# Kernel tuning notes

Measured on AMD Instinct MI355X. Metric: run time of the kernel, lower is better.

The kernel has to match this reference:

```python
import jax, jax.numpy as jnp
from jax import lax
import numpy as np

B, M = 16384, 200            # flattened batch (B*TT), tokens per observation
NUM_LAYERS, GW, GH = 22, 11, 11
CNN_CH, HIDDEN = 128, 512
ACTION_NVEC = (9, 10)

MAX_VEC = jnp.array([9.0, 1.0, 1.0, 10.0, 3.0, 254.0, 1.0, 1.0, 235.0, 8.0, 9.0,
                     250.0, 29.0, 1.0, 1.0, 8.0, 1.0, 1.0, 6.0, 3.0, 1.0, 2.0],
                    jnp.float32)[None, :, None, None]  # [1,22,1,1]


def setup_inputs() -> dict:
    key = jax.random.key(0)
    ks = jax.random.split(key, 16)
    # compose coords byte so x,y nibbles are valid grid indices (0..10)
    xs = jax.random.randint(ks[0], (B, M), 0, GW)
    ys = jax.random.randint(ks[1], (B, M), 0, GH)
    coords = xs * 16 + ys
    atr = jax.random.randint(ks[2], (B, M), 0, NUM_LAYERS)
    val = jax.random.randint(ks[3], (B, M), 0, 11)
    observations = jnp.stack([coords, atr, val], axis=-1).astype(jnp.int32)  # [B,M,3]

    def nrm(k, shape, std=0.02):
        return (jax.random.normal(k, shape, jnp.float32) * std)

    return {
        "observations": observations,
        "conv1_w": nrm(ks[4], (CNN_CH, NUM_LAYERS, 5, 5)),
        "conv1_b": jnp.zeros((CNN_CH,), jnp.float32),
        "conv2_w": nrm(ks[5], (CNN_CH, CNN_CH, 3, 3)),
        "conv2_b": jnp.zeros((CNN_CH,), jnp.float32),
        "fc_w": nrm(ks[6], (HIDDEN // 2, CNN_CH)),
        "fc_b": jnp.zeros((HIDDEN // 2,), jnp.float32),
        "self_w": nrm(ks[7], (HIDDEN // 2, NUM_LAYERS)),
        "self_b": jnp.zeros((HIDDEN // 2,), jnp.float32),
        "actor0_w": nrm(ks[8], (ACTION_NVEC[0], HIDDEN), std=0.01),
        "actor0_b": jnp.zeros((ACTION_NVEC[0],), jnp.float32),
        "actor1_w": nrm(ks[9], (ACTION_NVEC[1], HIDDEN), std=0.01),
        "actor1_b": jnp.zeros((ACTION_NVEC[1],), jnp.float32),
        "value_w": nrm(ks[10], (1, HIDDEN)),
        "value_b": jnp.zeros((1,), jnp.float32),
    }


def reference(observations, conv1_w, conv1_b, conv2_w, conv2_b, fc_w, fc_b,
              self_w, self_b, actor0_w, actor0_b, actor1_w, actor1_b,
              value_w, value_b):
    obs = jnp.where(observations == 255, 0, observations)
    coords = obs[..., 0]
    xs = (coords >> 4) & 15
    ys = coords & 15
    atr = obs[..., 1]
    vals = obs[..., 2].astype(jnp.float32)           # [B,M]
    Bt = obs.shape[0]
    b_idx = jnp.broadcast_to(jnp.arange(Bt)[:, None], vals.shape)
    # masked scatter into dense grid (all tokens valid after 255->0 clamp)
    box = jnp.zeros((Bt, NUM_LAYERS, GW, GH), jnp.float32)
    box = box.at[b_idx, atr, xs, ys].set(vals, mode="drop")
    feats = box / MAX_VEC                            # [B,22,11,11]

    self_f = jax.nn.relu(feats[:, :, 5, 5] @ self_w.T + self_b)  # [B,256]

    dn = ("NCHW", "OIHW", "NCHW")
    h = lax.conv_general_dilated(feats, conv1_w, (3, 3), "VALID", dimension_numbers=dn)
    h = jax.nn.relu(h + conv1_b[None, :, None, None])            # [B,128,3,3]
    h = lax.conv_general_dilated(h, conv2_w, (1, 1), "VALID", dimension_numbers=dn)
    h = jax.nn.relu(h + conv2_b[None, :, None, None])            # [B,128,1,1]
    h = h.reshape(Bt, -1)
    cnn_f = jax.nn.relu(h @ fc_w.T + fc_b)                       # [B,256]

    hidden = jnp.concatenate([self_f, cnn_f], axis=1)            # [B,512]
    logits0 = hidden @ actor0_w.T + actor0_b
    logits1 = hidden @ actor1_w.T + actor1_b
    value = hidden @ value_w.T + value_b
    return (logits0, logits1, value)
```

## Files before the change

kernel.cpp:

```cpp
#include <hip/hip_runtime.h>

typedef unsigned short u16;
typedef __attribute__((ext_vector_type(8))) short short8;
typedef __attribute__((ext_vector_type(4))) float f32x4;

#define MFMA16(a, b, c) __builtin_amdgcn_mfma_f32_16x16x32_bf16((a), (b), (c), 0, 0, 0)

__device__ __forceinline__ u16 f2bf(float f) {
    unsigned u = __float_as_uint(f);
    unsigned r = (u + 0x7FFFu + ((u >> 16) & 1u)) >> 16;
    return (u16)r;
}

__device__ const float MAXV[22] = {9.f, 1.f, 1.f, 10.f, 3.f, 254.f, 1.f, 1.f, 235.f, 8.f, 9.f,
                                   250.f, 29.f, 1.f, 1.f, 8.f, 1.f, 1.f, 6.f, 3.f, 1.f, 2.f};

__global__ void prep_kernel(
    const float* c1w, const float* c1b, const float* c2w, const float* c2b,
    const float* fcw, const float* fcb, const float* sfw, const float* sfb,
    const float* a0w, const float* a0b, const float* a1w, const float* a1b,
    const float* vw, const float* vb,
    u16* W1F, u16* W2F, u16* FCF, u16* SELFF, u16* HEADF, float* BIAS)
{
    int idx = blockIdx.x * 256 + threadIdx.x;
    if (idx < 73728) {
        int grp = idx >> 9, off = idx & 511;
        int g = grp / 18, ks = grp - g * 18;
        int l = off >> 3, e = off & 7;
        int n = g * 16 + (l & 15);
        int k = ks * 32 + ((l >> 4) << 3) + e;
        float v = 0.f;
        if (k < 550) { int c = k / 25; v = c1w[n * 550 + k] * (1.0f / MAXV[c]); }
        W1F[idx] = f2bf(v);
    } else if (idx < 221184) {
        int j = idx - 73728;
        int grp = j >> 9, off = j & 511;
        int g = grp / 36, ks = grp - g * 36;
        int l = off >> 3, e = off & 7;
        int oc = g * 16 + (l & 15);
        int k = ks * 32 + ((l >> 4) << 3) + e;
        W2F[j] = f2bf(c2w[oc * 1152 + (k & 127) * 9 + (k >> 7)]);
    } else if (idx < 253952) {
        int j = idx - 221184;
        int grp = j >> 9, off = j & 511;
        int g = grp >> 2, kc = grp & 3;
        int l = off >> 3, e = off & 7;
        int n = g * 16 + (l & 15);
        int k = kc * 32 + ((l >> 4) << 3) + e;
        FCF[j] = f2bf(fcw[n * 128 + k]);
    } else if (idx < 262144) {
        int j = idx - 253952;
        int g = j >> 9, off = j & 511;
        int l = off >> 3, e = off & 7;
        int n = g * 16 + (l & 15);
        int k = ((l >> 4) << 3) + e;
        float v = (k < 22) ? sfw[n * 22 + k] * (1.0f / MAXV[k]) : 0.f;
        SELFF[j] = f2bf(v);
    } else if (idx < 278528) {
        int j = idx - 262144;
        int grp = j >> 9, off = j & 511;
        int g = grp >> 4, ks = grp & 15;
        int l = off >> 3, e = off & 7;
        int n = g * 16 + (l & 15);
        int k = ks * 32 + ((l >> 4) << 3) + e;
        float v = 0.f;
        if (n < 9) v = a0w[n * 512 + k];
        else if (n < 19) v = a1w[(n - 9) * 512 + k];
        else if (n == 19) v = vw[k];
        HEADF[j] = f2bf(v);
    } else if (idx < 279328) {
        int j = idx - 278528;
        float v = 0.f;
        if (j < 128) v = c1b[j];
        else if (j < 256) v = c2b[j - 128];
        else if (j < 512) v = fcb[j - 256];
        else if (j < 768) v = sfb[j - 512];
        else {
            int j2 = j - 768;
            if (j2 < 9) v = a0b[j2]; else if (j2 < 19) v = a1b[j2 - 9]; else if (j2 == 19) v = vb[0];
        }
        BIAS[j] = v;
    }
}

__global__ __launch_bounds__(256, 3) void k12_kernel(
    const int* __restrict__ obs, const u16* __restrict__ W1F,
    const float* __restrict__ BIAS, u16* __restrict__ h1F, u16* __restrict__ s22g)
{
    __shared__ __align__(16) u16 Ablk[4 * 5328];
    __shared__ u16 s22[128];
    const int tid = threadIdx.x, w = tid >> 6, l = tid & 63;
    const int s0 = blockIdx.x * 4;
    const short8 z8 = {0, 0, 0, 0, 0, 0, 0, 0};

    const int* myobs = obs + (long)(s0 + w) * 600;
    int tk[4][3];
    #pragma unroll
    for (int r = 0; r < 4; ++r) {
        int m = r * 64 + l; m = m < 200 ? m : 0;
        tk[r][0] = myobs[m * 3]; tk[r][1] = myobs[m * 3 + 1]; tk[r][2] = myobs[m * 3 + 2];
    }
    if (l < 32) s22[w * 32 + l] = 0;

    u16* blk = Ablk + w * 5328;
    for (int i = l; i < 666; i += 64) *(short8*)(blk + i * 8) = z8;

    int* boxW = (int*)blk;
    int ce[4], en[4], ok[4], va[4], xa[4], ya[4], aa[4], win[4];
    #pragma unroll
    for (int r = 0; r < 4; ++r) {
        int m = r * 64 + l;
        int c = tk[r][0], a = tk[r][1], v = tk[r][2];
        c = (c == 255) ? 0 : c; a = (a == 255) ? 0 : a; v = (v == 255) ? 0 : v;
        int xs = (c >> 4) & 15, ys = c & 15;
        ok[r] = (m < 200) & ((unsigned)a < 22u) & (xs < 11) & (ys < 11);
        ce[r] = ok[r] ? (a * 121 + xs * 11 + ys) : 0;
        en[r] = ((m + 1) << 8) | (v & 255);
        va[r] = v; xa[r] = xs; ya[r] = ys; aa[r] = a;
        if (ok[r]) atomicMax(&boxW[ce[r]], en[r]);
    }
    __builtin_amdgcn_sched_barrier(0);
    #pragma unroll
    for (int r = 0; r < 4; ++r) win[r] = ok[r] & (boxW[ce[r]] == en[r]);
    __builtin_amdgcn_sched_barrier(0);
    for (int i = l; i < 666; i += 64) *(short8*)(blk + i * 8) = z8;
    __builtin_amdgcn_sched_barrier(0);
    #pragma unroll
    for (int r = 0; r < 4; ++r) {
        if (win[r]) {
            u16 bv = f2bf((float)va[r]);
            if (xa[r] == 5 && ya[r] == 5) s22[w * 32 + aa[r]] = bv;
            int bcol = aa[r] * 25;
            #pragma unroll
            for (int ox = 0; ox < 3; ++ox) {
                int kx = xa[r] - 3 * ox;
                if ((unsigned)kx > 4u) continue;
                #pragma unroll
                for (int oy = 0; oy < 3; ++oy) {
                    int ky = ya[r] - 3 * oy;
                    if ((unsigned)ky > 4u) continue;
                    int pos = ox * 3 + oy;
                    int row = w * 9 + pos;
                    int off = (((pos * 576 + bcol + kx * 5 + ky)) << 1) ^ ((row & 7) << 4);
                    *(u16*)((char*)blk + off) = bv;
                }
            }
        }
    }
    if (l < 32) s22g[(s0 + w) * 32 + l] = s22[w * 32 + l];
    __syncthreads();

    int addr[3][2];
    #pragma unroll
    for (int mt = 0; mt < 3; ++mt) {
        int row = mt * 16 + (l & 15);
        row = row < 36 ? row : 35;
        int ls = row / 9, pos = row - ls * 9;
        int koff = (l >> 4) << 3;
        addr[mt][0] = ls * 10656 + (((pos * 576 + koff) << 1) ^ ((row & 7) << 4));
        addr[mt][1] = ls * 10656 + (((pos * 576 + 32 + koff) << 1) ^ ((row & 7) << 4));
    }
    const u16* Wp0 = W1F + ((w * 2 + 0) * 18 << 9) + l * 8;
    const u16* Wp1 = W1F + ((w * 2 + 1) * 18 << 9) + l * 8;

    f32x4 acc[3][2];
    const f32x4 fz = {0.f, 0.f, 0.f, 0.f};
    #pragma unroll
    for (int i = 0; i < 3; ++i) { acc[i][0] = fz; acc[i][1] = fz; }

    short8 cb0 = *(const short8*)(Wp0);
    short8 cb1 = *(const short8*)(Wp1);
    short8 nb0 = *(const short8*)(Wp0 + 512);
    short8 nb1 = *(const short8*)(Wp1 + 512);
    __builtin_amdgcn_s_setprio(1);
    #pragma unroll
    for (int ks = 0; ks < 18; ++ks) {
        short8 t0 = cb0, t1 = cb1;
        if (ks < 16) {
            t0 = *(const short8*)(Wp0 + (ks + 2) * 512);
            t1 = *(const short8*)(Wp1 + (ks + 2) * 512);
        }
        short8 a0 = *(const short8*)((const char*)Ablk + addr[0][ks & 1] + (ks >> 1) * 128);
        short8 a1 = *(const short8*)((const char*)Ablk + addr[1][ks & 1] + (ks >> 1) * 128);
        short8 a2 = *(const short8*)((const char*)Ablk + addr[2][ks & 1] + (ks >> 1) * 128);
        acc[0][0] = MFMA16(a0, cb0, acc[0][0]);
        acc[0][1] = MFMA16(a0, cb1, acc[0][1]);
        acc[1][0] = MFMA16(a1, cb0, acc[1][0]);
        acc[1][1] = MFMA16(a1, cb1, acc[1][1]);
        acc[2][0] = MFMA16(a2, cb0, acc[2][0]);
        acc[2][1] = MFMA16(a2, cb1, acc[2][1]);
        cb0 = nb0; cb1 = nb1; nb0 = t0; nb1 = t1;
    }
    __builtin_amdgcn_s_setprio(0);
    __syncthreads();

    u16* R = Ablk;
    #pragma unroll
    for (int mt = 0; mt < 3; ++mt) {
        #pragma unroll
        for (int nt = 0; nt < 2; ++nt) {
            int col = w * 32 + nt * 16 + (l & 15);
            float bias = BIAS[col];
            int hif = nt * 2 + ((l & 15) >> 3);
            int ef = l & 7;
            #pragma unroll
            for (int r = 0; r < 4; ++r) {
                int row = mt * 16 + ((l >> 4) << 2) + r;
                if (row < 36) {
                    int ds = row / 9;
                    int pos = row - ds * 9;
                    int ks = pos * 4 + w;
                    float v = acc[mt][nt][r] + bias;
                    v = v > 0.f ? v : 0.f;
                    R[(ks * 16 + hif * 4 + ds) * 8 + ef] = f2bf(v);
                }
            }
        }
    }
    __syncthreads();
    {
        const long Cbase = (long)(s0 >> 4) * 18432 + (s0 & 15) * 8;
        #pragma unroll
        for (int q = 0; q < 3; ++q) {
            int slot = tid + q * 256;
            if (slot < 576) {
                int ks = slot >> 4, lf = slot & 15;
                *(short8*)(h1F + Cbase + ks * 512 + (lf >> 2) * 128 + (lf & 3) * 8) =
                    *(const short8*)(R + slot * 8);
            }
        }
    }
}

__global__ __launch_bounds__(256, 4) void k3_kernel(
    const u16* __restrict__ h1F, const u16* __restrict__ s22g,
    const u16* __restrict__ W2F, const u16* __restrict__ FCF,
    const u16* __restrict__ SELFF, const u16* __restrict__ HEADF,
    const float* __restrict__ BIAS, float* __restrict__ out, int B)
{
    __shared__ __align__(16) u16 A3[16 * 136];
    __shared__ __align__(16) u16 HID[16 * 520];
    const int tid = threadIdx.x, w = tid >> 6, l = tid & 63;
    const int s0 = blockIdx.x * 16;
    const float* c2b = BIAS + 128;
    const float* fcb = BIAS + 256;
    const float* sfb = BIAS + 512;
    const float* hdb = BIAS + 768;
    const f32x4 fz = {0.f, 0.f, 0.f, 0.f};

    const u16* Ap  = h1F + (long)blockIdx.x * 18432 + l * 8;
    const u16* B0p = W2F + ((w * 2 + 0) * 36 << 9) + l * 8;
    const u16* B1p = W2F + ((w * 2 + 1) * 36 << 9) + l * 8;
    f32x4 acc0 = fz, acc1 = fz;
    short8 pa[3], pb0[3], pb1[3];
    #pragma unroll
    for (int d = 0; d < 3; ++d) {
        pa[d]  = *(const short8*)(Ap + d * 512);
        pb0[d] = *(const short8*)(B0p + d * 512);
        pb1[d] = *(const short8*)(B1p + d * 512);
    }
    __builtin_amdgcn_s_setprio(1);
    #pragma unroll
    for (int g = 0; g < 12; ++g) {
        #pragma unroll
        for (int d = 0; d < 3; ++d) {
            int ks = g * 3 + d;
            short8 a = pa[d], b0 = pb0[d], b1 = pb1[d];
            if (ks < 33) {
                pa[d]  = *(const short8*)(Ap + (ks + 3) * 512);
                pb0[d] = *(const short8*)(B0p + (ks + 3) * 512);
                pb1[d] = *(const short8*)(B1p + (ks + 3) * 512);
            }
            acc0 = MFMA16(a, b0, acc0);
            acc1 = MFMA16(a, b1, acc1);
        }
    }
    __builtin_amdgcn_s_setprio(0);
    {
        #pragma unroll
        for (int nt = 0; nt < 2; ++nt) {
            int col = w * 32 + nt * 16 + (l & 15);
            float bias = c2b[col];
            const f32x4& a4 = nt ? acc1 : acc0;
            #pragma unroll
            for (int r = 0; r < 4; ++r) {
                int row = ((l >> 4) << 2) + r;
                float v = a4[r] + bias; v = v > 0.f ? v : 0.f;
                A3[row * 136 + col] = f2bf(v);
            }
        }
    }
    __syncthreads();

    f32x4 acc8[4];
    #pragma unroll
    for (int j = 0; j < 4; ++j) acc8[j] = fz;
    #pragma unroll
    for (int kc = 0; kc < 4; ++kc) {
        short8 bf[4];
        #pragma unroll
        for (int nt = 0; nt < 4; ++nt)
            bf[nt] = *(const short8*)(FCF + (((w * 4 + nt) * 4 + kc) << 9) + l * 8);
        short8 a = *(const short8*)(A3 + (l & 15) * 136 + kc * 32 + ((l >> 4) << 3));
        #pragma unroll
        for (int nt = 0; nt < 4; ++nt) acc8[nt] = MFMA16(a, bf[nt], acc8[nt]);
    }
    #pragma unroll
    for (int nt = 0; nt < 4; ++nt) {
        int col = w * 64 + nt * 16 + (l & 15);
        float bias = fcb[col];
        #pragma unroll
        for (int r = 0; r < 4; ++r) {
            int row = ((l >> 4) << 2) + r;
            float v = acc8[nt][r] + bias; v = v > 0.f ? v : 0.f;
            HID[row * 520 + 256 + col] = f2bf(v);
        }
    }

    {
        f32x4 acc9[4];
        #pragma unroll
        for (int j = 0; j < 4; ++j) acc9[j] = fz;
        short8 bs[4];
        #pragma unroll
        for (int nt = 0; nt < 4; ++nt)
            bs[nt] = *(const short8*)(SELFF + ((w * 4 + nt) << 9) + l * 8);
        short8 a = *(const short8*)(s22g + (s0 + (l & 15)) * 32 + ((l >> 4) << 3));
        #pragma unroll
        for (int nt = 0; nt < 4; ++nt) acc9[nt] = MFMA16(a, bs[nt], acc9[nt]);
        #pragma unroll
        for (int nt = 0; nt < 4; ++nt) {
            int col = w * 64 + nt * 16 + (l & 15);
            float bias = sfb[col];
            #pragma unroll
            for (int r = 0; r < 4; ++r) {
                int row = ((l >> 4) << 2) + r;
                float v = acc9[nt][r] + bias; v = v > 0.f ? v : 0.f;
                HID[row * 520 + col] = f2bf(v);
            }
        }
    }
    __syncthreads();

    if (w < 2) {
        f32x4 hacc = fz;
        #pragma unroll
        for (int ks = 0; ks < 16; ++ks) {
            short8 a = *(const short8*)(HID + (l & 15) * 520 + ks * 32 + ((l >> 4) << 3));
            short8 b = *(const short8*)(HEADF + ((w * 16 + ks) << 9) + l * 8);
            hacc = MFMA16(a, b, hacc);
        }
        #pragma unroll
        for (int r = 0; r < 4; ++r) {
            int srow = s0 + ((l >> 4) << 2) + r;
            int col = w * 16 + (l & 15);
            float v = hacc[r] + hdb[col];
            if (col < 9) out[(long)srow * 9 + col] = v;
            else if (col < 19) out[(long)B * 9 + (long)srow * 10 + (col - 9)] = v;
            else if (col == 19) out[(long)B * 19 + srow] = v;
        }
    }
}

extern "C" void kernel_launch(void* const* d_in, const int* in_sizes, int n_in,
                              void* d_out, int out_size, void* d_ws, size_t ws_size,
                              hipStream_t stream)
{
    const int*   obs = (const int*)d_in[0];
    const float* c1w = (const float*)d_in[1];
    const float* c1b = (const float*)d_in[2];
    const float* c2w = (const float*)d_in[3];
    const float* c2b = (const float*)d_in[4];
    const float* fcw = (const float*)d_in[5];
    const float* fcb = (const float*)d_in[6];
    const float* sfw = (const float*)d_in[7];
    const float* sfb = (const float*)d_in[8];
    const float* a0w = (const float*)d_in[9];
    const float* a0b = (const float*)d_in[10];
    const float* a1w = (const float*)d_in[11];
    const float* a1b = (const float*)d_in[12];
    const float* vw  = (const float*)d_in[13];
    const float* vb  = (const float*)d_in[14];
    const int B = in_sizes[0] / 600;

    char* ws = (char*)d_ws;
    u16*   W1F   = (u16*)(ws + 0);
    u16*   W2F   = (u16*)(ws + 147456);
    u16*   FCF   = (u16*)(ws + 442368);
    u16*   SELFF = (u16*)(ws + 507904);
    u16*   HEADF = (u16*)(ws + 524288);
    float* BIAS  = (float*)(ws + 557056);
    u16*   s22g  = (u16*)(ws + 560256);
    u16*   h1F   = (u16*)(ws + 560256 + (size_t)B * 64);

    prep_kernel<<<1092, 256, 0, stream>>>(c1w, c1b, c2w, c2b, fcw, fcb, sfw, sfb,
                                          a0w, a0b, a1w, a1b, vw, vb,
                                          W1F, W2F, FCF, SELFF, HEADF, BIAS);
    k12_kernel<<<B / 4, 256, 0, stream>>>(obs, W1F, BIAS, h1F, s22g);
    k3_kernel<<<B / 16, 256, 0, stream>>>(h1F, s22g, W2F, FCF, SELFF, HEADF, BIAS,
                                          (float*)d_out, B);
}
```

Before: 79.31 us.

## Persist conv1 weights in registers across samples and split conv2 into its own kernel

The conv1 kernel now handles 16 samples per block in a four-iteration loop. It keeps all of its B-fragment weights in registers (36 short8) instead of re-streaming them per block, and prefetches the next group's observations. Outputs go straight to global memory with scattered 2-byte stores rather than through an LDS staging pass. Conv2 moves into a new kernel that processes 32 samples per block so each weight load is reused twice, and its output goes to a global buffer that a third kernel reads for the FC and head layers. This adds a kernel launch and a global round-trip, and the higher register pressure lowers the occupancy target to 2.

```diff
diff --git a/kernel.cpp b/kernel.cpp
--- a/kernel.cpp
+++ b/kernel.cpp
@@ -83,72 +83,26 @@
     }
 }
 
-__global__ __launch_bounds__(256, 3) void k12_kernel(
+__global__ __launch_bounds__(256, 2) void k12_kernel(
     const int* __restrict__ obs, const u16* __restrict__ W1F,
     const float* __restrict__ BIAS, u16* __restrict__ h1F, u16* __restrict__ s22g)
 {
     __shared__ __align__(16) u16 Ablk[4 * 5328];
     __shared__ u16 s22[128];
     const int tid = threadIdx.x, w = tid >> 6, l = tid & 63;
-    const int s0 = blockIdx.x * 4;
+    const int sbase = blockIdx.x * 16;
     const short8 z8 = {0, 0, 0, 0, 0, 0, 0, 0};
-
-    const int* myobs = obs + (long)(s0 + w) * 600;
-    int tk[4][3];
-    #pragma unroll
-    for (int r = 0; r < 4; ++r) {
-        int m = r * 64 + l; m = m < 200 ? m : 0;
-        tk[r][0] = myobs[m * 3]; tk[r][1] = myobs[m * 3 + 1]; tk[r][2] = myobs[m * 3 + 2];
-    }
-    if (l < 32) s22[w * 32 + l] = 0;
-
     u16* blk = Ablk + w * 5328;
-    for (int i = l; i < 666; i += 64) *(short8*)(blk + i * 8) = z8;
-
     int* boxW = (int*)blk;
-    int ce[4], en[4], ok[4], va[4], xa[4], ya[4], aa[4], win[4];
-    #pragma unroll
-    for (int r = 0; r < 4; ++r) {
-        int m = r * 64 + l;
-        int c = tk[r][0], a = tk[r][1], v = tk[r][2];
-        c = (c == 255) ? 0 : c; a = (a == 255) ? 0 : a; v = (v == 255) ? 0 : v;
-        int xs = (c >> 4) & 15, ys = c & 15;
-        ok[r] = (m < 200) & ((unsigned)a < 22u) & (xs < 11) & (ys < 11);
-        ce[r] = ok[r] ? (a * 121 + xs * 11 + ys) : 0;
-        en[r] = ((m + 1) << 8) | (v & 255);
-        va[r] = v; xa[r] = xs; ya[r] = ys; aa[r] = a;
-        if (ok[r]) atomicMax(&boxW[ce[r]], en[r]);
-    }
-    __builtin_amdgcn_sched_barrier(0);
-    #pragma unroll
-    for (int r = 0; r < 4; ++r) win[r] = ok[r] & (boxW[ce[r]] == en[r]);
-    __builtin_amdgcn_sched_barrier(0);
-    for (int i = l; i < 666; i += 64) *(short8*)(blk + i * 8) = z8;
-    __builtin_amdgcn_sched_barrier(0);
-    #pragma unroll
-    for (int r = 0; r < 4; ++r) {
-        if (win[r]) {
-            u16 bv = f2bf((float)va[r]);
-            if (xa[r] == 5 && ya[r] == 5) s22[w * 32 + aa[r]] = bv;
-            int bcol = aa[r] * 25;
-            #pragma unroll
-            for (int ox = 0; ox < 3; ++ox) {
-                int kx = xa[r] - 3 * ox;
-                if ((unsigned)kx > 4u) continue;
-                #pragma unroll
-                for (int oy = 0; oy < 3; ++oy) {
-                    int ky = ya[r] - 3 * oy;
-                    if ((unsigned)ky > 4u) continue;
-                    int pos = ox * 3 + oy;
-                    int row = w * 9 + pos;
-                    int off = (((pos * 576 + bcol + kx * 5 + ky)) << 1) ^ ((row & 7) << 4);
-                    *(u16*)((char*)blk + off) = bv;
-                }
-            }
-        }
-    }
-    if (l < 32) s22g[(s0 + w) * 32 + l] = s22[w * 32 + l];
-    __syncthreads();
+
+    short8 bfr[36];
+    #pragma unroll
+    for (int nt = 0; nt < 2; ++nt)
+        #pragma unroll
+        for (int ks = 0; ks < 18; ++ks)
+            bfr[nt * 18 + ks] = *(const short8*)(W1F + (((w * 2 + nt) * 18 + ks) << 9) + l * 8);
+    #pragma unroll
+    for (int i = 0; i < 36; ++i) asm volatile("" : "+v"(bfr[i]));
 
     int addr[3][2];
     #pragma unroll
@@ -160,150 +114,214 @@
         addr[mt][0] = ls * 10656 + (((pos * 576 + koff) << 1) ^ ((row & 7) << 4));
         addr[mt][1] = ls * 10656 + (((pos * 576 + 32 + koff) << 1) ^ ((row & 7) << 4));
     }
-    const u16* Wp0 = W1F + ((w * 2 + 0) * 18 << 9) + l * 8;
-    const u16* Wp1 = W1F + ((w * 2 + 1) * 18 << 9) + l * 8;
-
-    f32x4 acc[3][2];
+    const int col0 = w * 32 + (l & 15);
+    const float bias0 = BIAS[col0], bias1 = BIAS[col0 + 16];
+
+    int tkc[4][3], tkn[4][3];
+    {
+        const int* myobs = obs + (long)(sbase + w) * 600;
+        #pragma unroll
+        for (int r = 0; r < 4; ++r) {
+            int m = r * 64 + l; m = m < 200 ? m : 0;
+            tkc[r][0] = myobs[m * 3]; tkc[r][1] = myobs[m * 3 + 1]; tkc[r][2] = myobs[m * 3 + 2];
+        }
+    }
+
+    #pragma clang loop unroll(disable)
+    for (int it = 0; it < 4; ++it) {
+        const int s0it = sbase + it * 4;
+        for (int i = l; i < 666; i += 64) *(short8*)(blk + i * 8) = z8;
+        if (l < 32) s22[w * 32 + l] = 0;
+        int ce[4], en[4], okm = 0;
+        #pragma unroll
+        for (int r = 0; r < 4; ++r) {
+            int m = r * 64 + l;
+            int c = tkc[r][0], a = tkc[r][1], v = tkc[r][2];
+            c = (c == 255) ? 0 : c; a = (a == 255) ? 0 : a; v = (v == 255) ? 0 : v;
+            int xs = (c >> 4) & 15, ys = c & 15;
+            int ok = (m < 200) & ((unsigned)a < 22u) & (xs < 11) & (ys < 11);
+            okm |= ok << r;
+            ce[r] = ok ? (a * 121 + xs * 11 + ys) : 0;
+            en[r] = ((m + 1) << 8) | (v & 255);
+            if (ok) atomicMax(&boxW[ce[r]], en[r]);
+        }
+        __builtin_amdgcn_sched_barrier(0);
+        int winm = 0;
+        #pragma unroll
+        for (int r = 0; r < 4; ++r)
+            if (((okm >> r) & 1) && boxW[ce[r]] == en[r]) winm |= 1 << r;
+        __builtin_amdgcn_sched_barrier(0);
+        for (int i = l; i < 666; i += 64) *(short8*)(blk + i * 8) = z8;
+        __builtin_amdgcn_sched_barrier(0);
+        #pragma unroll
+        for (int r = 0; r < 4; ++r) {
+            if ((winm >> r) & 1) {
+                int c = tkc[r][0], a = tkc[r][1], v = tkc[r][2];
+                c = (c == 255) ? 0 : c; a = (a == 255) ? 0 : a; v = (v == 255) ? 0 : v;
+                int xs = (c >> 4) & 15, ys = c & 15;
+                u16 bv = f2bf((float)v);
+                if (xs == 5 && ys == 5) s22[w * 32 + a] = bv;
+                int bcol = a * 25;
+                #pragma unroll
+                for (int ox = 0; ox < 3; ++ox) {
+                    int kx = xs - 3 * ox;
+                    if ((unsigned)kx > 4u) continue;
+                    #pragma unroll
+                    for (int oy = 0; oy < 3; ++oy) {
+                        int ky = ys - 3 * oy;
+                        if ((unsigned)ky > 4u) continue;
+                        int pos = ox * 3 + oy;
+                        int row = w * 9 + pos;
+                        int off = ((pos * 576 + bcol + kx * 5 + ky) << 1) ^ ((row & 7) << 4);
+                        *(u16*)((char*)blk + off) = bv;
+                    }
+                }
+            }
+        }
+        if (it < 3) {
+            const int* myobs = obs + (long)(sbase + (it + 1) * 4 + w) * 600;
+            #pragma unroll
+            for (int r = 0; r < 4; ++r) {
+                int m = r * 64 + l; m = m < 200 ? m : 0;
+                tkn[r][0] = myobs[m * 3]; tkn[r][1] = myobs[m * 3 + 1]; tkn[r][2] = myobs[m * 3 + 2];
+            }
+        }
+        if (l < 32) s22g[(s0it + w) * 32 + l] = s22[w * 32 + l];
+        __syncthreads();
+
+        f32x4 acc[3][2];
+        const f32x4 fz = {0.f, 0.f, 0.f, 0.f};
+        #pragma unroll
+        for (int i = 0; i < 3; ++i) { acc[i][0] = fz; acc[i][1] = fz; }
+        __builtin_amdgcn_s_setprio(1);
+        #pragma unroll
+        for (int ks = 0; ks < 18; ++ks) {
+            short8 a0 = *(const short8*)((const char*)Ablk + addr[0][ks & 1] + (ks >> 1) * 128);
+            short8 a1 = *(const short8*)((const char*)Ablk + addr[1][ks & 1] + (ks >> 1) * 128);
+            short8 a2 = *(const short8*)((const char*)Ablk + addr[2][ks & 1] + (ks >> 1) * 128);
+            acc[0][0] = MFMA16(a0, bfr[ks], acc[0][0]);
+            acc[0][1] = MFMA16(a0, bfr[18 + ks], acc[0][1]);
+            acc[1][0] = MFMA16(a1, bfr[ks], acc[1][0]);
+            acc[1][1] = MFMA16(a1, bfr[18 + ks], acc[1][1]);
+            acc[2][0] = MFMA16(a2, bfr[ks], acc[2][0]);
+            acc[2][1] = MFMA16(a2, bfr[18 + ks], acc[2][1]);
+        }
+        __builtin_amdgcn_s_setprio(0);
+        __syncthreads();
+
+        #pragma unroll
+        for (int mt = 0; mt < 3; ++mt) {
+            #pragma unroll
+            for (int nt = 0; nt < 2; ++nt) {
+                int col = col0 + nt * 16;
+                float bias = nt ? bias1 : bias0;
+                #pragma unroll
+                for (int r = 0; r < 4; ++r) {
+                    int row = mt * 16 + ((l >> 4) << 2) + r;
+                    if (row < 36) {
+                        int ls = row / 9, pos = row - ls * 9;
+                        int s = s0it + ls;
+                        float v = acc[mt][nt][r] + bias;
+                        v = v > 0.f ? v : 0.f;
+                        long ad = (long)(s >> 4) * 18432 + (pos * 4 + w) * 512 +
+                                  (s & 15) * 8 + (((col & 31) >> 3) << 7) + (col & 7);
+                        h1F[ad] = f2bf(v);
+                    }
+                }
+            }
+        }
+        if (it < 3) {
+            #pragma unroll
+            for (int r = 0; r < 4; ++r) {
+                tkc[r][0] = tkn[r][0]; tkc[r][1] = tkn[r][1]; tkc[r][2] = tkn[r][2];
+            }
+        }
+    }
+}
+
+__global__ __launch_bounds__(256, 2) void k3a_kernel(
+    const u16* __restrict__ h1F, const u16* __restrict__ W2F,
+    const float* __restrict__ BIAS, u16* __restrict__ a3F)
+{
+    const int tid = threadIdx.x, w = tid >> 6, l = tid & 63;
+    const int sb = blockIdx.x * 2, s0 = blockIdx.x * 32;
+    const float* c2b = BIAS + 128;
     const f32x4 fz = {0.f, 0.f, 0.f, 0.f};
-    #pragma unroll
-    for (int i = 0; i < 3; ++i) { acc[i][0] = fz; acc[i][1] = fz; }
-
-    short8 cb0 = *(const short8*)(Wp0);
-    short8 cb1 = *(const short8*)(Wp1);
-    short8 nb0 = *(const short8*)(Wp0 + 512);
-    short8 nb1 = *(const short8*)(Wp1 + 512);
+    f32x4 acc[2][2];
+    acc[0][0] = fz; acc[0][1] = fz; acc[1][0] = fz; acc[1][1] = fz;
+
+    const u16* A0p = h1F + (long)(sb + 0) * 18432 + l * 8;
+    const u16* A1p = h1F + (long)(sb + 1) * 18432 + l * 8;
+    const u16* B0p = W2F + ((w * 2 + 0) * 36 << 9) + l * 8;
+    const u16* B1p = W2F + ((w * 2 + 1) * 36 << 9) + l * 8;
+
+    short8 ca0 = *(const short8*)(A0p), ca1 = *(const short8*)(A1p);
+    short8 cb0 = *(const short8*)(B0p), cb1 = *(const short8*)(B1p);
+    short8 na0 = *(const short8*)(A0p + 512), na1 = *(const short8*)(A1p + 512);
+    short8 nb0 = *(const short8*)(B0p + 512), nb1 = *(const short8*)(B1p + 512);
     __builtin_amdgcn_s_setprio(1);
     #pragma unroll
-    for (int ks = 0; ks < 18; ++ks) {
-        short8 t0 = cb0, t1 = cb1;
-        if (ks < 16) {
-            t0 = *(const short8*)(Wp0 + (ks + 2) * 512);
-            t1 = *(const short8*)(Wp1 + (ks + 2) * 512);
-        }
-        short8 a0 = *(const short8*)((const char*)Ablk + addr[0][ks & 1] + (ks >> 1) * 128);
-        short8 a1 = *(const short8*)((const char*)Ablk + addr[1][ks & 1] + (ks >> 1) * 128);
-        short8 a2 = *(const short8*)((const char*)Ablk + addr[2][ks & 1] + (ks >> 1) * 128);
-        acc[0][0] = MFMA16(a0, cb0, acc[0][0]);
-        acc[0][1] = MFMA16(a0, cb1, acc[0][1]);
-        acc[1][0] = MFMA16(a1, cb0, acc[1][0]);
-        acc[1][1] = MFMA16(a1, cb1, acc[1][1]);
-        acc[2][0] = MFMA16(a2, cb0, acc[2][0]);
-        acc[2][1] = MFMA16(a2, cb1, acc[2][1]);
-        cb0 = nb0; cb1 = nb1; nb0 = t0; nb1 = t1;
+    for (int ks = 0; ks < 36; ++ks) {
+        short8 t0 = ca0, t1 = ca1, t2 = cb0, t3 = cb1;
+        if (ks < 34) {
+            t0 = *(const short8*)(A0p + (ks + 2) * 512);
+            t1 = *(const short8*)(A1p + (ks + 2) * 512);
+            t2 = *(const short8*)(B0p + (ks + 2) * 512);
+            t3 = *(const short8*)(B1p + (ks + 2) * 512);
+        }
+        acc[0][0] = MFMA16(ca0, cb0, acc[0][0]);
+        acc[0][1] = MFMA16(ca0, cb1, acc[0][1]);
+        acc[1][0] = MFMA16(ca1, cb0, acc[1][0]);
+        acc[1][1] = MFMA16(ca1, cb1, acc[1][1]);
+        ca0 = na0; ca1 = na1; cb0 = nb0; cb1 = nb1;
+        na0 = t0; na1 = t1; nb0 = t2; nb1 = t3;
     }
     __builtin_amdgcn_s_setprio(0);
-    __syncthreads();
-
-    u16* R = Ablk;
-    #pragma unroll
-    for (int mt = 0; mt < 3; ++mt) {
+
+    #pragma unroll
+    for (int mt = 0; mt < 2; ++mt) {
         #pragma unroll
         for (int nt = 0; nt < 2; ++nt) {
             int col = w * 32 + nt * 16 + (l & 15);
-            float bias = BIAS[col];
-            int hif = nt * 2 + ((l & 15) >> 3);
-            int ef = l & 7;
+            float bias = c2b[col];
             #pragma unroll
             for (int r = 0; r < 4; ++r) {
                 int row = mt * 16 + ((l >> 4) << 2) + r;
-                if (row < 36) {
-                    int ds = row / 9;
-                    int pos = row - ds * 9;
-                    int ks = pos * 4 + w;
-                    float v = acc[mt][nt][r] + bias;
-                    v = v > 0.f ? v : 0.f;
-                    R[(ks * 16 + hif * 4 + ds) * 8 + ef] = f2bf(v);
-                }
-            }
-        }
-    }
-    __syncthreads();
-    {
-        const long Cbase = (long)(s0 >> 4) * 18432 + (s0 & 15) * 8;
-        #pragma unroll
-        for (int q = 0; q < 3; ++q) {
-            int slot = tid + q * 256;
-            if (slot < 576) {
-                int ks = slot >> 4, lf = slot & 15;
-                *(short8*)(h1F + Cbase + ks * 512 + (lf >> 2) * 128 + (lf & 3) * 8) =
-                    *(const short8*)(R + slot * 8);
-            }
-        }
-    }
-}
-
-__global__ __launch_bounds__(256, 4) void k3_kernel(
-    const u16* __restrict__ h1F, const u16* __restrict__ s22g,
-    const u16* __restrict__ W2F, const u16* __restrict__ FCF,
-    const u16* __restrict__ SELFF, const u16* __restrict__ HEADF,
-    const float* __restrict__ BIAS, float* __restrict__ out, int B)
+                int s = s0 + row;
+                float v = acc[mt][nt][r] + bias; v = v > 0.f ? v : 0.f;
+                long ad = (long)(s >> 4) * 2048 + (col >> 5) * 512 +
+                          (s & 15) * 8 + (((col >> 3) & 3) << 7) + (col & 7);
+                a3F[ad] = f2bf(v);
+            }
+        }
+    }
+}
+
+__global__ __launch_bounds__(256, 4) void k3b_kernel(
+    const u16* __restrict__ a3F, const u16* __restrict__ s22g,
+    const u16* __restrict__ FCF, const u16* __restrict__ SELFF,
+    const u16* __restrict__ HEADF, const float* __restrict__ BIAS,
+    float* __restrict__ out, int B)
 {
-    __shared__ __align__(16) u16 A3[16 * 136];
     __shared__ __align__(16) u16 HID[16 * 520];
     const int tid = threadIdx.x, w = tid >> 6, l = tid & 63;
     const int s0 = blockIdx.x * 16;
-    const float* c2b = BIAS + 128;
     const float* fcb = BIAS + 256;
     const float* sfb = BIAS + 512;
     const float* hdb = BIAS + 768;
     const f32x4 fz = {0.f, 0.f, 0.f, 0.f};
 
-    const u16* Ap  = h1F + (long)blockIdx.x * 18432 + l * 8;
-    const u16* B0p = W2F + ((w * 2 + 0) * 36 << 9) + l * 8;
-    const u16* B1p = W2F + ((w * 2 + 1) * 36 << 9) + l * 8;
-    f32x4 acc0 = fz, acc1 = fz;
-    short8 pa[3], pb0[3], pb1[3];
-    #pragma unroll
-    for (int d = 0; d < 3; ++d) {
-        pa[d]  = *(const short8*)(Ap + d * 512);
-        pb0[d] = *(const short8*)(B0p + d * 512);
-        pb1[d] = *(const short8*)(B1p + d * 512);
-    }
-    __builtin_amdgcn_s_setprio(1);
-    #pragma unroll
-    for (int g = 0; g < 12; ++g) {
-        #pragma unroll
-        for (int d = 0; d < 3; ++d) {
-            int ks = g * 3 + d;
-            short8 a = pa[d], b0 = pb0[d], b1 = pb1[d];
-            if (ks < 33) {
-                pa[d]  = *(const short8*)(Ap + (ks + 3) * 512);
-                pb0[d] = *(const short8*)(B0p + (ks + 3) * 512);
-                pb1[d] = *(const short8*)(B1p + (ks + 3) * 512);
-            }
-            acc0 = MFMA16(a, b0, acc0);
-            acc1 = MFMA16(a, b1, acc1);
-        }
-    }
-    __builtin_amdgcn_s_setprio(0);
-    {
-        #pragma unroll
-        for (int nt = 0; nt < 2; ++nt) {
-            int col = w * 32 + nt * 16 + (l & 15);
-            float bias = c2b[col];
-            const f32x4& a4 = nt ? acc1 : acc0;
-            #pragma unroll
-            for (int r = 0; r < 4; ++r) {
-                int row = ((l >> 4) << 2) + r;
-                float v = a4[r] + bias; v = v > 0.f ? v : 0.f;
-                A3[row * 136 + col] = f2bf(v);
-            }
-        }
-    }
-    __syncthreads();
-
     f32x4 acc8[4];
     #pragma unroll
     for (int j = 0; j < 4; ++j) acc8[j] = fz;
     #pragma unroll
     for (int kc = 0; kc < 4; ++kc) {
-        short8 bf[4];
-        #pragma unroll
-        for (int nt = 0; nt < 4; ++nt)
-            bf[nt] = *(const short8*)(FCF + (((w * 4 + nt) * 4 + kc) << 9) + l * 8);
-        short8 a = *(const short8*)(A3 + (l & 15) * 136 + kc * 32 + ((l >> 4) << 3));
-        #pragma unroll
-        for (int nt = 0; nt < 4; ++nt) acc8[nt] = MFMA16(a, bf[nt], acc8[nt]);
+        short8 a = *(const short8*)(a3F + (long)blockIdx.x * 2048 + kc * 512 + l * 8);
+        #pragma unroll
+        for (int nt = 0; nt < 4; ++nt) {
+            short8 bf = *(const short8*)(FCF + (((w * 4 + nt) * 4 + kc) << 9) + l * 8);
+            acc8[nt] = MFMA16(a, bf, acc8[nt]);
+        }
     }
     #pragma unroll
     for (int nt = 0; nt < 4; ++nt) {
@@ -321,13 +339,12 @@
         f32x4 acc9[4];
         #pragma unroll
         for (int j = 0; j < 4; ++j) acc9[j] = fz;
-        short8 bs[4];
-        #pragma unroll
-        for (int nt = 0; nt < 4; ++nt)
-            bs[nt] = *(const short8*)(SELFF + ((w * 4 + nt) << 9) + l * 8);
         short8 a = *(const short8*)(s22g + (s0 + (l & 15)) * 32 + ((l >> 4) << 3));
         #pragma unroll
-        for (int nt = 0; nt < 4; ++nt) acc9[nt] = MFMA16(a, bs[nt], acc9[nt]);
+        for (int nt = 0; nt < 4; ++nt) {
+            short8 bs = *(const short8*)(SELFF + ((w * 4 + nt) << 9) + l * 8);
+            acc9[nt] = MFMA16(a, bs, acc9[nt]);
+        }
         #pragma unroll
         for (int nt = 0; nt < 4; ++nt) {
             int col = w * 64 + nt * 16 + (l & 15);
@@ -392,11 +409,13 @@
     float* BIAS  = (float*)(ws + 557056);
     u16*   s22g  = (u16*)(ws + 560256);
     u16*   h1F   = (u16*)(ws + 560256 + (size_t)B * 64);
+    u16*   a3F   = (u16*)(ws + 560256 + (size_t)B * 64 + (size_t)B * 2304);
 
     prep_kernel<<<1092, 256, 0, stream>>>(c1w, c1b, c2w, c2b, fcw, fcb, sfw, sfb,
                                           a0w, a0b, a1w, a1b, vw, vb,
                                           W1F, W2F, FCF, SELFF, HEADF, BIAS);
-    k12_kernel<<<B / 4, 256, 0, stream>>>(obs, W1F, BIAS, h1F, s22g);
-    k3_kernel<<<B / 16, 256, 0, stream>>>(h1F, s22g, W2F, FCF, SELFF, HEADF, BIAS,
-                                          (float*)d_out, B);
-}
+    k12_kernel<<<B / 16, 256, 0, stream>>>(obs, W1F, BIAS, h1F, s22g);
+    k3a_kernel<<<B / 32, 256, 0, stream>>>(h1F, W2F, BIAS, a3F);
+    k3b_kernel<<<B / 16, 256, 0, stream>>>(a3F, s22g, FCF, SELFF, HEADF, BIAS,
+                                           (float*)d_out, B);
+}
```

New measurement: 126.6 us. 1.6x slower.
